# Performance work log

Hardware: AMD Instinct MI355X
Metric: run time of the kernel (lower is better)

## Reference

```python
import jax, jax.numpy as jnp
import numpy as np

D_MODEL = 512
HIDDEN_MULT = 4
D_FF = D_MODEL * HIDDEN_MULT
B, L = 4, 1024


def setup_inputs() -> dict:
    key = jax.random.key(0)
    ks = jax.random.split(key, 7)
    s1 = 1.0 / np.sqrt(D_MODEL)
    s2 = 1.0 / np.sqrt(D_FF)
    return {
        "x": jax.random.normal(ks[0], (B, L, D_MODEL), dtype=jnp.float32),
        "W1": jax.random.uniform(ks[1], (D_FF, D_MODEL), minval=-s1, maxval=s1, dtype=jnp.float32),
        "b1": jax.random.uniform(ks[2], (D_FF,), minval=-s1, maxval=s1, dtype=jnp.float32),
        "W2": jax.random.uniform(ks[3], (D_MODEL, D_FF), minval=-s2, maxval=s2, dtype=jnp.float32),
        "b2": jax.random.uniform(ks[4], (D_MODEL,), minval=-s2, maxval=s2, dtype=jnp.float32),
        "Lambda_raw_F": jax.random.uniform(ks[5], (D_FF, D_MODEL), minval=-3.0, maxval=3.0, dtype=jnp.float32),
        "Gamma_F": jax.random.uniform(ks[6], (D_FF, D_MODEL), minval=-0.5 * s1, maxval=0.5 * s1, dtype=jnp.float32),
    }


def _stp_forward(x, W1, b1, W2, b2, Lambda_raw_F, Gamma_F):
    # x: (B, L, D)
    retention = 1.0 - jax.nn.sigmoid(Lambda_raw_F)  # (d_ff, D)
    gamma = Gamma_F
    # static contribution of W1: (B, L, d_ff)
    static_h = jnp.einsum('bld,fd->blf', x, W1) + b1

    def step(F_state, inputs):
        # F_state: (B, d_ff, D); x_t: (B, D); sh_t: (B, d_ff)
        x_t, sh_t = inputs
        h_pre = sh_t + jnp.einsum('bfd,bd->bf', F_state, x_t)
        h = jax.nn.gelu(h_pre, approximate=False)
        out = jnp.einsum('bf,df->bd', h, W2) + b2
        # Hebbian outer-product update
        F_new = retention[None] * F_state + gamma[None] * (h_pre[:, :, None] * x_t[:, None, :])
        return F_new, out

    F0 = jnp.zeros((x.shape[0], W1.shape[0], W1.shape[1]), dtype=x.dtype)
    xs = (jnp.swapaxes(x, 0, 1), jnp.swapaxes(static_h, 0, 1))  # (L, B, ...)
    _, ys = jax.lax.scan(step, F0, xs)
    return jnp.swapaxes(ys, 0, 1)  # (B, L, D)


def reference(x, W1, b1, W2, b2, Lambda_raw_F, Gamma_F):
    return _stp_forward(x, W1, b1, W2, b2, Lambda_raw_F, Gamma_F)
```

## Files before the change

### kernel.cpp

```cpp
#include <hip/hip_runtime.h>
#include <cstdint>

#define DM   512
#define DFF  2048
#define BSZ  4
#define LSEQ 1024

__device__ __forceinline__ float4 f4fma(float4 a, float4 b, float4 c) {
    return make_float4(fmaf(a.x, b.x, c.x), fmaf(a.y, b.y, c.y),
                       fmaf(a.z, b.z, c.z), fmaf(a.w, b.w, c.w));
}
__device__ __forceinline__ float4 f4mul(float4 a, float4 b) {
    return make_float4(a.x * b.x, a.y * b.y, a.z * b.z, a.w * b.w);
}

__global__ __launch_bounds__(256, 4)
void stp_scan(const float* __restrict__ x,
              const float* __restrict__ W1,
              const float* __restrict__ b1,
              const float* __restrict__ Lam,
              const float* __restrict__ Gam,
              float* __restrict__ hbuf)
{
    const int tid  = threadIdx.x;
    const int lane = tid & 63;
    const int wid  = tid >> 6;
    const int j    = lane & 31;
    const int g    = lane >> 5;
    const int b    = blockIdx.x >> 8;
    const int fbase = (blockIdx.x & 255) << 3;
    const int f    = fbase + (wid << 1) + g;

    const float4* __restrict__ x4 =
        reinterpret_cast<const float4*>(x + (size_t)b * LSEQ * DM);

    float4 FW[4], R[4], G[4], WR[4];
    {
        const float4* lr = reinterpret_cast<const float4*>(Lam + (size_t)f * DM);
        const float4* gr = reinterpret_cast<const float4*>(Gam + (size_t)f * DM);
        const float4* wr = reinterpret_cast<const float4*>(W1  + (size_t)f * DM);
        #pragma unroll
        for (int k = 0; k < 4; ++k) {
            const int idx = j + 32 * k;
            float4 lv = lr[idx];
            float4 rv;
            rv.x = 1.0f / (1.0f + expf(lv.x));
            rv.y = 1.0f / (1.0f + expf(lv.y));
            rv.z = 1.0f / (1.0f + expf(lv.z));
            rv.w = 1.0f / (1.0f + expf(lv.w));
            R[k] = rv;
            G[k] = gr[idx];
            float4 wv = wr[idx];
            FW[k] = wv;
            WR[k].x = wv.x * (1.0f - rv.x);
            WR[k].y = wv.y * (1.0f - rv.y);
            WR[k].z = wv.z * (1.0f - rv.z);
            WR[k].w = wv.w * (1.0f - rv.w);
        }
    }
    const float b1v = b1[f];

    float* __restrict__ hout = hbuf + (size_t)b * LSEQ * DFF + f;

    float4 xr[4];
    #pragma unroll
    for (int k = 0; k < 4; ++k) xr[k] = x4[j + 32 * k];

    #pragma unroll 2
    for (int t = 0; t < LSEQ; ++t) {
        const int tn = (t + 1 < LSEQ) ? (t + 1) : t;
        float4 xn[4];
        #pragma unroll
        for (int k = 0; k < 4; ++k) xn[k] = x4[tn * 128 + j + 32 * k];

        float4 acc = make_float4(0.f, 0.f, 0.f, 0.f);
        #pragma unroll
        for (int k = 0; k < 4; ++k) acc = f4fma(FW[k], xr[k], acc);
        float p = (acc.x + acc.y) + (acc.z + acc.w);

        p += __shfl_xor(p, 1);
        p += __shfl_xor(p, 2);
        p += __shfl_xor(p, 4);
        p += __shfl_xor(p, 8);
        p += __shfl_xor(p, 16);

        const float hp = p + b1v;

        const float hg = 0.5f * hp * (1.0f + erff(hp * 0.70710678118654752f));
        if (j == 0) hout[(size_t)t * DFF] = hg;

        #pragma unroll
        for (int k = 0; k < 4; ++k) {
            float4 gx = f4mul(G[k], xr[k]);
            float4 s;
            s.x = fmaf(gx.x, hp, WR[k].x);
            s.y = fmaf(gx.y, hp, WR[k].y);
            s.z = fmaf(gx.z, hp, WR[k].z);
            s.w = fmaf(gx.w, hp, WR[k].w);
            FW[k] = f4fma(R[k], FW[k], s);
        }

        #pragma unroll
        for (int k = 0; k < 4; ++k) xr[k] = xn[k];
    }
}

__global__ __launch_bounds__(256)
void gemm_nt_bias(const float* __restrict__ A,
                  const float* __restrict__ Bm,
                  const float* __restrict__ bias,
                  float* __restrict__ C,
                  int M, int N, int K)
{
    __shared__ float As[16][68];
    __shared__ float Bs[16][68];

    const int tid = threadIdx.x;
    const int tx  = tid & 15;
    const int ty  = tid >> 4;
    const int row0 = blockIdx.y * 64;
    const int col0 = blockIdx.x * 64;

    const int lr = tid >> 2;
    const int lk = (tid & 3) << 2;

    const float* Aptr = A  + (size_t)(row0 + lr) * K + lk;
    const float* Bptr = Bm + (size_t)(col0 + lr) * K + lk;

    float acc[4][4] = {};
    float4 av = *reinterpret_cast<const float4*>(Aptr);
    float4 bv = *reinterpret_cast<const float4*>(Bptr);

    const int NT = K >> 4;
    for (int kt = 0; kt < NT; ++kt) {
        __syncthreads();
        As[lk + 0][lr] = av.x; As[lk + 1][lr] = av.y;
        As[lk + 2][lr] = av.z; As[lk + 3][lr] = av.w;
        Bs[lk + 0][lr] = bv.x; Bs[lk + 1][lr] = bv.y;
        Bs[lk + 2][lr] = bv.z; Bs[lk + 3][lr] = bv.w;
        __syncthreads();

        if (kt + 1 < NT) {
            av = *reinterpret_cast<const float4*>(Aptr + (kt + 1) * 16);
            bv = *reinterpret_cast<const float4*>(Bptr + (kt + 1) * 16);
        }

        #pragma unroll
        for (int k = 0; k < 16; ++k) {
            float4 a = *reinterpret_cast<const float4*>(&As[k][ty * 4]);
            float4 bb = *reinterpret_cast<const float4*>(&Bs[k][tx * 4]);
            acc[0][0] = fmaf(a.x, bb.x, acc[0][0]);
            acc[0][1] = fmaf(a.x, bb.y, acc[0][1]);
            acc[0][2] = fmaf(a.x, bb.z, acc[0][2]);
            acc[0][3] = fmaf(a.x, bb.w, acc[0][3]);
            acc[1][0] = fmaf(a.y, bb.x, acc[1][0]);
            acc[1][1] = fmaf(a.y, bb.y, acc[1][1]);
            acc[1][2] = fmaf(a.y, bb.z, acc[1][2]);
            acc[1][3] = fmaf(a.y, bb.w, acc[1][3]);
            acc[2][0] = fmaf(a.z, bb.x, acc[2][0]);
            acc[2][1] = fmaf(a.z, bb.y, acc[2][1]);
            acc[2][2] = fmaf(a.z, bb.z, acc[2][2]);
            acc[2][3] = fmaf(a.z, bb.w, acc[2][3]);
            acc[3][0] = fmaf(a.w, bb.x, acc[3][0]);
            acc[3][1] = fmaf(a.w, bb.y, acc[3][1]);
            acc[3][2] = fmaf(a.w, bb.z, acc[3][2]);
            acc[3][3] = fmaf(a.w, bb.w, acc[3][3]);
        }
    }

    const float4 bb = *reinterpret_cast<const float4*>(&bias[col0 + tx * 4]);
    #pragma unroll
    for (int i = 0; i < 4; ++i) {
        float4 o;
        o.x = acc[i][0] + bb.x;
        o.y = acc[i][1] + bb.y;
        o.z = acc[i][2] + bb.z;
        o.w = acc[i][3] + bb.w;
        *reinterpret_cast<float4*>(&C[(size_t)(row0 + ty * 4 + i) * N + col0 + tx * 4]) = o;
    }
}

extern "C" void kernel_launch(void* const* d_in, const int* in_sizes, int n_in,
                              void* d_out, int out_size, void* d_ws, size_t ws_size,
                              hipStream_t stream)
{
    const float* x   = (const float*)d_in[0];
    const float* W1  = (const float*)d_in[1];
    const float* b1  = (const float*)d_in[2];
    const float* W2  = (const float*)d_in[3];
    const float* b2  = (const float*)d_in[4];
    const float* Lam = (const float*)d_in[5];
    const float* Gam = (const float*)d_in[6];
    float* out  = (float*)d_out;
    float* hbuf = (float*)d_ws;

    stp_scan<<<dim3(BSZ * (DFF / 8)), dim3(256), 0, stream>>>(x, W1, b1, Lam, Gam, hbuf);

    dim3 g2(DM / 64, (BSZ * LSEQ) / 64);
    gemm_nt_bias<<<g2, dim3(256), 0, stream>>>(hbuf, W2, b2, out, BSZ * LSEQ, DM, DFF);
}
```

Measured before the change: 915.2 us.

## Precompute static W1 projection via GEMM and simplify scan to zero-init state

The static x·W1ᵀ+b1 projection is moved out of the recurrent scan into a separate tiled GEMM that writes pre-activations to the workspace. The scan now starts F from zero without a folded W1 term. Each wave handles one feature row across 64 lanes, reads the precomputed value per step, and writes h_pre back in place. GELU is applied in its own elementwise pass before the output GEMM. This removes the per-step W1/retention-fold arithmetic and raises occupancy, at the cost of an extra global load inside the serial loop, more shuffle reductions per feature, and two extra kernel launches with full passes over the hidden buffer.

New measurement: 1.067 ms. 1.17x slower.

```diff
diff --git a/kernel.cpp b/kernel.cpp
--- a/kernel.cpp
+++ b/kernel.cpp
@@ -14,94 +14,93 @@
     return make_float4(a.x * b.x, a.y * b.y, a.z * b.z, a.w * b.w);
 }
 
-__global__ __launch_bounds__(256, 4)
+__global__ __launch_bounds__(256, 8)
 void stp_scan(const float* __restrict__ x,
-              const float* __restrict__ W1,
-              const float* __restrict__ b1,
               const float* __restrict__ Lam,
               const float* __restrict__ Gam,
               float* __restrict__ hbuf)
 {
-    const int tid  = threadIdx.x;
-    const int lane = tid & 63;
-    const int wid  = tid >> 6;
-    const int j    = lane & 31;
-    const int g    = lane >> 5;
-    const int b    = blockIdx.x >> 8;
-    const int fbase = (blockIdx.x & 255) << 3;
-    const int f    = fbase + (wid << 1) + g;
+    const int lane = threadIdx.x & 63;
+    const int wid  = __builtin_amdgcn_readfirstlane(threadIdx.x) >> 6;
+    const int b    = blockIdx.x >> 9;
+    const int f    = ((blockIdx.x & 511) << 2) + wid;
 
     const float4* __restrict__ x4 =
         reinterpret_cast<const float4*>(x + (size_t)b * LSEQ * DM);
-
-    float4 FW[4], R[4], G[4], WR[4];
+    float* __restrict__ hrow = hbuf + (size_t)b * LSEQ * DFF + f;
+
+    float4 F0 = make_float4(0.f, 0.f, 0.f, 0.f);
+    float4 F1 = make_float4(0.f, 0.f, 0.f, 0.f);
+    float4 R0, R1, G0, G1;
     {
         const float4* lr = reinterpret_cast<const float4*>(Lam + (size_t)f * DM);
         const float4* gr = reinterpret_cast<const float4*>(Gam + (size_t)f * DM);
-        const float4* wr = reinterpret_cast<const float4*>(W1  + (size_t)f * DM);
-        #pragma unroll
-        for (int k = 0; k < 4; ++k) {
-            const int idx = j + 32 * k;
-            float4 lv = lr[idx];
-            float4 rv;
-            rv.x = 1.0f / (1.0f + expf(lv.x));
-            rv.y = 1.0f / (1.0f + expf(lv.y));
-            rv.z = 1.0f / (1.0f + expf(lv.z));
-            rv.w = 1.0f / (1.0f + expf(lv.w));
-            R[k] = rv;
-            G[k] = gr[idx];
-            float4 wv = wr[idx];
-            FW[k] = wv;
-            WR[k].x = wv.x * (1.0f - rv.x);
-            WR[k].y = wv.y * (1.0f - rv.y);
-            WR[k].z = wv.z * (1.0f - rv.z);
-            WR[k].w = wv.w * (1.0f - rv.w);
-        }
-    }
-    const float b1v = b1[f];
-
-    float* __restrict__ hout = hbuf + (size_t)b * LSEQ * DFF + f;
-
-    float4 xr[4];
-    #pragma unroll
-    for (int k = 0; k < 4; ++k) xr[k] = x4[j + 32 * k];
-
-    #pragma unroll 2
-    for (int t = 0; t < LSEQ; ++t) {
-        const int tn = (t + 1 < LSEQ) ? (t + 1) : t;
-        float4 xn[4];
-        #pragma unroll
-        for (int k = 0; k < 4; ++k) xn[k] = x4[tn * 128 + j + 32 * k];
-
-        float4 acc = make_float4(0.f, 0.f, 0.f, 0.f);
-        #pragma unroll
-        for (int k = 0; k < 4; ++k) acc = f4fma(FW[k], xr[k], acc);
-        float p = (acc.x + acc.y) + (acc.z + acc.w);
-
-        p += __shfl_xor(p, 1);
-        p += __shfl_xor(p, 2);
-        p += __shfl_xor(p, 4);
-        p += __shfl_xor(p, 8);
-        p += __shfl_xor(p, 16);
-
-        const float hp = p + b1v;
-
-        const float hg = 0.5f * hp * (1.0f + erff(hp * 0.70710678118654752f));
-        if (j == 0) hout[(size_t)t * DFF] = hg;
-
-        #pragma unroll
-        for (int k = 0; k < 4; ++k) {
-            float4 gx = f4mul(G[k], xr[k]);
-            float4 s;
-            s.x = fmaf(gx.x, hp, WR[k].x);
-            s.y = fmaf(gx.y, hp, WR[k].y);
-            s.z = fmaf(gx.z, hp, WR[k].z);
-            s.w = fmaf(gx.w, hp, WR[k].w);
-            FW[k] = f4fma(R[k], FW[k], s);
-        }
-
-        #pragma unroll
-        for (int k = 0; k < 4; ++k) xr[k] = xn[k];
+        float4 l0 = lr[lane], l1 = lr[lane + 64];
+        R0.x = 1.0f / (1.0f + expf(l0.x));
+        R0.y = 1.0f / (1.0f + expf(l0.y));
+        R0.z = 1.0f / (1.0f + expf(l0.z));
+        R0.w = 1.0f / (1.0f + expf(l0.w));
+        R1.x = 1.0f / (1.0f + expf(l1.x));
+        R1.y = 1.0f / (1.0f + expf(l1.y));
+        R1.z = 1.0f / (1.0f + expf(l1.z));
+        R1.w = 1.0f / (1.0f + expf(l1.w));
+        G0 = gr[lane];
+        G1 = gr[lane + 64];
+    }
+
+#define STP_STEP(T, X0, X1)                                               \
+    {                                                                     \
+        float4 a = f4fma(F0, (X0), make_float4(0.f, 0.f, 0.f, 0.f));      \
+        a = f4fma(F1, (X1), a);                                           \
+        float p = (a.x + a.y) + (a.z + a.w);                              \
+        p += __shfl_xor(p, 1);                                            \
+        p += __shfl_xor(p, 2);                                            \
+        p += __shfl_xor(p, 4);                                            \
+        p += __shfl_xor(p, 8);                                            \
+        p += __shfl_xor(p, 16);                                           \
+        p += __shfl_xor(p, 32);                                           \
+        const float hp = p + hrow[(size_t)(T) * DFF];                     \
+        if (lane == 0) hrow[(size_t)(T) * DFF] = hp;                      \
+        float4 gx0 = f4mul(G0, (X0));                                     \
+        float4 gx1 = f4mul(G1, (X1));                                     \
+        float4 rf0 = f4mul(R0, F0);                                       \
+        float4 rf1 = f4mul(R1, F1);                                       \
+        F0.x = fmaf(gx0.x, hp, rf0.x);                                    \
+        F0.y = fmaf(gx0.y, hp, rf0.y);                                    \
+        F0.z = fmaf(gx0.z, hp, rf0.z);                                    \
+        F0.w = fmaf(gx0.w, hp, rf0.w);                                    \
+        F1.x = fmaf(gx1.x, hp, rf1.x);                                    \
+        F1.y = fmaf(gx1.y, hp, rf1.y);                                    \
+        F1.z = fmaf(gx1.z, hp, rf1.z);                                    \
+        F1.w = fmaf(gx1.w, hp, rf1.w);                                    \
+    }
+
+    float4 xA0 = x4[lane], xA1 = x4[lane + 64];
+    #pragma unroll 1
+    for (int t = 0; t < LSEQ; t += 2) {
+        float4 xB0 = x4[(t + 1) * 128 + lane];
+        float4 xB1 = x4[(t + 1) * 128 + 64 + lane];
+        STP_STEP(t, xA0, xA1);
+        const int t2 = (t + 2 < LSEQ) ? (t + 2) : (LSEQ - 1);
+        xA0 = x4[t2 * 128 + lane];
+        xA1 = x4[t2 * 128 + 64 + lane];
+        STP_STEP(t + 1, xB0, xB1);
+    }
+#undef STP_STEP
+}
+
+__global__ __launch_bounds__(256)
+void gelu_inplace(float4* __restrict__ p, int n4)
+{
+    int i = blockIdx.x * blockDim.x + threadIdx.x;
+    const int stride = gridDim.x * blockDim.x;
+    for (; i < n4; i += stride) {
+        float4 v = p[i];
+        v.x = 0.5f * v.x * (1.0f + erff(v.x * 0.70710678118654752f));
+        v.y = 0.5f * v.y * (1.0f + erff(v.y * 0.70710678118654752f));
+        v.z = 0.5f * v.z * (1.0f + erff(v.z * 0.70710678118654752f));
+        v.w = 0.5f * v.w * (1.0f + erff(v.w * 0.70710678118654752f));
+        p[i] = v;
     }
 }
 
@@ -194,8 +193,16 @@
     float* out  = (float*)d_out;
     float* hbuf = (float*)d_ws;
 
-    stp_scan<<<dim3(BSZ * (DFF / 8)), dim3(256), 0, stream>>>(x, W1, b1, Lam, Gam, hbuf);
-
-    dim3 g2(DM / 64, (BSZ * LSEQ) / 64);
-    gemm_nt_bias<<<g2, dim3(256), 0, stream>>>(hbuf, W2, b2, out, BSZ * LSEQ, DM, DFF);
-}
+    const int M = BSZ * LSEQ;
+
+    gemm_nt_bias<<<dim3(DFF / 64, M / 64), dim3(256), 0, stream>>>(
+        x, W1, b1, hbuf, M, DFF, DM);
+
+    stp_scan<<<dim3(BSZ * (DFF / 4)), dim3(256), 0, stream>>>(x, Lam, Gam, hbuf);
+
+    gelu_inplace<<<dim3(2048), dim3(256), 0, stream>>>(
+        reinterpret_cast<float4*>(hbuf), M * DFF / 4);
+
+    gemm_nt_bias<<<dim3(DM / 64, M / 64), dim3(256), 0, stream>>>(
+        hbuf, W2, b2, out, M, DM, DFF);
+}
```
